# Performance work log

Hardware: AMD Instinct MI355X
Metric: run time of the kernel (lower is better)

Reference implementation:

```python
import jax, jax.numpy as jnp
import numpy as np

B, T, N, D, H, MH = 4, 16, 128, 16, 64, 128  # batch, timesteps, nodes, n_in_node, n_hid, msg_hid


def setup_inputs() -> dict:
    key = jax.random.key(0)
    ks = jax.random.split(key, 24)
    s = 0.1
    inp = {
        'A': jax.random.uniform(ks[0], (B, N, N), dtype=jnp.float32),
        'X': jax.random.normal(ks[1], (B, T, N, D), dtype=jnp.float32),
        'W_msg1': s * jax.random.normal(ks[2], (2 * H, MH), dtype=jnp.float32),
        'b_msg1': s * jax.random.normal(ks[3], (MH,), dtype=jnp.float32),
        'W_msg2': s * jax.random.normal(ks[4], (MH, H), dtype=jnp.float32),
        'b_msg2': s * jax.random.normal(ks[5], (H,), dtype=jnp.float32),
        'W_ir': s * jax.random.normal(ks[6], (D, H), dtype=jnp.float32),
        'b_ir': s * jax.random.normal(ks[7], (H,), dtype=jnp.float32),
        'W_ii': s * jax.random.normal(ks[8], (D, H), dtype=jnp.float32),
        'b_ii': s * jax.random.normal(ks[9], (H,), dtype=jnp.float32),
        'W_in': s * jax.random.normal(ks[10], (D, H), dtype=jnp.float32),
        'b_in': s * jax.random.normal(ks[11], (H,), dtype=jnp.float32),
        'W_hr': s * jax.random.normal(ks[12], (H, H), dtype=jnp.float32),
        'W_hi': s * jax.random.normal(ks[13], (H, H), dtype=jnp.float32),
        'W_hh': s * jax.random.normal(ks[14], (H, H), dtype=jnp.float32),
        'W_o1': s * jax.random.normal(ks[15], (H, H), dtype=jnp.float32),
        'b_o1': s * jax.random.normal(ks[16], (H,), dtype=jnp.float32),
        'W_o2': s * jax.random.normal(ks[17], (H, H), dtype=jnp.float32),
        'b_o2': s * jax.random.normal(ks[18], (H,), dtype=jnp.float32),
        'W_o3': s * jax.random.normal(ks[19], (H, D), dtype=jnp.float32),
        'b_o3': s * jax.random.normal(ks[20], (D,), dtype=jnp.float32),
        'log_sigma': jnp.log(jnp.float32(0.1)),
    }
    return inp


def reference(A, X, W_msg1, b_msg1, W_msg2, b_msg2, W_ir, b_ir, W_ii, b_ii,
              W_in, b_in, W_hr, W_hi, W_hh, W_o1, b_o1, W_o2, b_o2, W_o3,
              b_o3, log_sigma):
    Bv, Tv, Nv, Dv = X.shape
    Hv = W_hr.shape[0]
    # project_adjacency: symmetrize, zero diag, clamp to [0,1]
    A = (A + jnp.swapaxes(A, -1, -2)) * 0.5
    A = A * (1.0 - jnp.eye(Nv, dtype=A.dtype))
    A = jnp.clip(A, 0.0, 1.0)
    # split msg_fc1 into sender / receiver halves (cat([senders, receivers]) @ W)
    W1s, W1r = W_msg1[:Hv], W_msg1[Hv:]

    def step(carry, xs):
        hidden, total = carry
        x_t, x_next = xs  # [B,N,D]
        # message passing on hidden state: msg1[b,i,j] = tanh(h_i@W1s + h_j@W1r + b)
        hs = hidden @ W1s                      # [B,N,MH] sender part
        hr = hidden @ W1r + b_msg1             # [B,N,MH] receiver part
        m1 = jnp.tanh(hs[:, :, None, :] + hr[:, None, :, :])  # [B,N,N,MH]
        msg = jnp.tanh(m1 @ W_msg2 + b_msg2)   # [B,N,N,H]
        # weight by soft adjacency, sum over senders i -> agg at receiver j
        agg = jnp.einsum('bij,bijh->bjh', A, msg)  # [B,N,H]
        # GRU-style gating
        r = jax.nn.sigmoid(x_t @ W_ir + b_ir + agg @ W_hr)
        i = jax.nn.sigmoid(x_t @ W_ii + b_ii + agg @ W_hi)
        n = jnp.tanh(x_t @ W_in + b_in + r * (agg @ W_hh))
        hidden_new = (1.0 - i) * n + i * hidden
        # output MLP with residual
        p1 = jax.nn.relu(hidden_new @ W_o1 + b_o1)
        p2 = jax.nn.relu(p1 @ W_o2 + b_o2)
        pred = x_t + (p2 @ W_o3 + b_o3)
        # gaussian log-likelihood
        sigma = jnp.exp(log_sigma)
        mse = jnp.sum((x_next - pred) ** 2)
        const = Nv * Dv * Bv * jnp.log(sigma * jnp.sqrt(2.0 * jnp.pi))
        total = total - (mse / (2.0 * sigma ** 2) + const)
        return (hidden_new, total), pred

    hidden0 = jnp.zeros((Bv, Nv, Hv), dtype=X.dtype)
    xs = (jnp.swapaxes(X[:, :-1], 0, 1), jnp.swapaxes(X[:, 1:], 0, 1))  # time-major
    (_, loglik), preds = jax.lax.scan(step, (hidden0, jnp.float32(0.0)), xs)
    X_pred = jnp.swapaxes(preds, 0, 1)  # [B, T-1, N, D]
    return X_pred, loglik
```

## Files before the change

kernel.cpp:

```cpp
#include <hip/hip_runtime.h>

#define NBLK 512

#define OFF_HS   0
#define OFF_PART 65536
#define OFF_SYNC 66048
#define OFF_BF   66560

#define BW2F 0
#define BWIR 8192
#define BWII 9216
#define BWIN 10240
#define BWHR 11264
#define BWHI 15360
#define BWHH 19456
#define BWO1 23552
#define BWO2 27648
#define BWO3 31744
#define BW1S 32768

#define INIT_TOTAL (32768 + 512 + 49152)

typedef __attribute__((ext_vector_type(8))) __bf16 bf16x8;
typedef __attribute__((ext_vector_type(4))) float f32x4;
union frag_u { bf16x8 v; unsigned short s[8]; int4 q; };
union ldu { int4 q; unsigned short s[8]; };

__device__ __forceinline__ unsigned short f2b(float x) {
  unsigned int u = __float_as_uint(x);
  u += 0x7fffu + ((u >> 16) & 1u);
  return (unsigned short)(u >> 16);
}
__device__ __forceinline__ float b2f(unsigned short u) {
  return __uint_as_float(((unsigned int)u) << 16);
}
__device__ __forceinline__ float fast_tanh(float x) {
  float e = __builtin_amdgcn_exp2f(x * 2.8853900817779268f);
  return 1.0f - 2.0f * __builtin_amdgcn_rcpf(e + 1.0f);
}
__device__ __forceinline__ float fast_sigmoid(float x) {
  float e = __builtin_amdgcn_exp2f(x * -1.4426950408889634f);
  return __builtin_amdgcn_rcpf(1.0f + e);
}
__device__ __forceinline__ void st_coh_u32(unsigned* p, unsigned v) {
  __hip_atomic_store(p, v, __ATOMIC_RELAXED, __HIP_MEMORY_SCOPE_AGENT);
}
__device__ __forceinline__ void st_coh_i32(int* p, int v) {
  __hip_atomic_store(p, v, __ATOMIC_RELAXED, __HIP_MEMORY_SCOPE_AGENT);
}

__global__ void init_kernel(const float* __restrict__ W_msg2,
                            const float* __restrict__ W_ir, const float* __restrict__ W_ii,
                            const float* __restrict__ W_in,
                            const float* __restrict__ W_hr, const float* __restrict__ W_hi,
                            const float* __restrict__ W_hh,
                            const float* __restrict__ W_o1, const float* __restrict__ W_o2,
                            const float* __restrict__ W_o3,
                            const float* __restrict__ W_msg1, float* __restrict__ ws) {
  int idx = blockIdx.x * 256 + threadIdx.x;
  unsigned short* bw = (unsigned short*)(ws + OFF_BF);
  if (idx < 32768) { ws[OFF_HS + idx] = 0.0f; return; }
  idx -= 32768;
  if (idx < 512) { ((int*)(ws + OFF_SYNC))[idx] = 0; return; }
  idx -= 512;
  if (idx < 8192) {
    int f = idx >> 9, l = (idx >> 3) & 63, jj = idx & 7;
    int kc = f >> 2, nt = f & 3;
    int k = kc * 32 + ((l >> 4) << 3) + jj;
    int n = (nt << 4) + (l & 15);
    bw[BW2F + idx] = f2b(W_msg2[k * 64 + n]);
    return;
  }
  idx -= 8192;
  if (idx < 1024) { bw[BWIR + idx] = f2b(W_ir[idx]); return; }
  idx -= 1024;
  if (idx < 1024) { bw[BWII + idx] = f2b(W_ii[idx]); return; }
  idx -= 1024;
  if (idx < 1024) { bw[BWIN + idx] = f2b(W_in[idx]); return; }
  idx -= 1024;
  if (idx < 4096) { bw[BWHR + idx] = f2b(W_hr[idx]); return; }
  idx -= 4096;
  if (idx < 4096) { bw[BWHI + idx] = f2b(W_hi[idx]); return; }
  idx -= 4096;
  if (idx < 4096) { bw[BWHH + idx] = f2b(W_hh[idx]); return; }
  idx -= 4096;
  if (idx < 4096) { bw[BWO1 + idx] = f2b(W_o1[idx]); return; }
  idx -= 4096;
  if (idx < 4096) { bw[BWO2 + idx] = f2b(W_o2[idx]); return; }
  idx -= 4096;
  if (idx < 1024) { bw[BWO3 + idx] = f2b(W_o3[idx]); return; }
  idx -= 1024;
  if (idx < 16384) { bw[BW1S + idx] = f2b(W_msg1[idx]); return; }
}

__launch_bounds__(256, 2)
__global__ void step_all_kernel(const float* __restrict__ A, const float* __restrict__ X,
                                const float* __restrict__ b_msg1, const float* __restrict__ b_msg2,
                                const float* __restrict__ b_ir, const float* __restrict__ b_ii,
                                const float* __restrict__ b_in,
                                const float* __restrict__ b_o1, const float* __restrict__ b_o2,
                                const float* __restrict__ b_o3,
                                float* __restrict__ ws, float* __restrict__ out) {
  const int tid = threadIdx.x;
  const int bj = blockIdx.x;
  const int b = bj >> 7, j = bj & 127;
  const int wave = tid >> 6, lane = tid & 63;
  const unsigned short* bw = (const unsigned short*)(ws + OFF_BF);
  unsigned short* hs16 = (unsigned short*)(ws + OFF_HS);
  int* flags = (int*)(ws + OFF_SYNC);

  __shared__ unsigned short lds_gate[12288];
  __shared__ unsigned short lds_w1[16384];
  __shared__ unsigned short lds_out[9216];
  __shared__ __align__(16) float sh_hr[128];
  __shared__ __align__(16) float sh_Ar[128];
  __shared__ float sh_aggw[4][64];
  __shared__ float sh_agg[64];
  __shared__ float sh_x[16];
  __shared__ float sh_hid[64];
  __shared__ float sh_pre[4][64];
  __shared__ int sh_w01;

  {
    const int4* src = (const int4*)(bw + BWHR);
    int4* dst = (int4*)lds_gate;
    for (int i = tid; i < 1536; i += 256) dst[i] = src[i];
    const int4* s2 = (const int4*)(bw + BW1S);
    int4* d2 = (int4*)lds_w1;
    for (int i = tid; i < 2048; i += 256) d2[i] = s2[i];
    const int4* s3 = (const int4*)(bw + BWO1);
    int4* d3 = (int4*)lds_out;
    for (int i = tid; i < 1152; i += 256) d3[i] = s3[i];
  }
  if (tid < 128) {
    float a1 = A[(b << 14) + (j << 7) + tid];
    float a2 = A[(b << 14) + (tid << 7) + j];
    float v = 0.5f * (a1 + a2);
    v = (tid == j) ? 0.0f : v;
    sh_Ar[tid] = fminf(fmaxf(v, 0.0f), 1.0f);
    sh_hr[tid] = b_msg1[tid];
  } else if (tid < 192) {
    sh_hid[tid - 128] = 0.0f;
  }
  if (tid == 0) sh_w01 = 0;

  frag_u Bf[16];
  const int4* bw2 = (const int4*)bw;
#pragma unroll
  for (int f = 0; f < 16; ++f) Bf[f].q = bw2[f * 64 + lane];
  float b2v[4];
#pragma unroll
  for (int nt = 0; nt < 4; ++nt) b2v[nt] = b_msg2[nt * 16 + (lane & 15)];
  float my_bias = 0.0f;
  if (wave == 0) my_bias = b_ir[lane];
  else if (wave == 1) my_bias = b_ii[lane];
  else if (wave == 3) my_bias = b_in[lane];
  const float bm1a = b_msg1[lane], bm1b = b_msg1[lane + 64];
  const float bo1 = b_o1[lane], bo2 = b_o2[lane];
  const float bo3 = (lane < 16) ? b_o3[lane] : 0.0f;
  float macc = 0.0f;

  const int lane15 = lane & 15;
  const int k0 = (lane >> 4) << 3;
  __syncthreads();

  for (int t = 0; t < 15; ++t) {
    const int par = t & 1;
    const unsigned short* hs_cur = hs16 + par * 65536;
    unsigned short* hs_nxt = hs16 + (par ^ 1) * 65536;

    if (tid < 16) sh_x[tid] = X[(((b << 4) + t) << 11) + (j << 4) + tid];

    ldu va[8];
    {
      const unsigned short* p0 = hs_cur + (((b << 7) + (wave << 5) + lane15) << 7) + k0;
      const unsigned short* p1 = p0 + 2048;
      asm volatile(
          "global_load_dwordx4 %0, %8, off sc0 sc1\n\t"
          "global_load_dwordx4 %1, %8, off offset:64 sc0 sc1\n\t"
          "global_load_dwordx4 %2, %8, off offset:128 sc0 sc1\n\t"
          "global_load_dwordx4 %3, %8, off offset:192 sc0 sc1\n\t"
          "global_load_dwordx4 %4, %9, off sc0 sc1\n\t"
          "global_load_dwordx4 %5, %9, off offset:64 sc0 sc1\n\t"
          "global_load_dwordx4 %6, %9, off offset:128 sc0 sc1\n\t"
          "global_load_dwordx4 %7, %9, off offset:192 sc0 sc1\n\t"
          "s_waitcnt vmcnt(0)"
          : "=&v"(va[0].q), "=&v"(va[1].q), "=&v"(va[2].q), "=&v"(va[3].q),
            "=&v"(va[4].q), "=&v"(va[5].q), "=&v"(va[6].q), "=&v"(va[7].q)
          : "v"(p0), "v"(p1)
          : "memory");
    }

    float part[4] = {0.f, 0.f, 0.f, 0.f};
#pragma unroll
    for (int c = 0; c < 2; ++c) {
      f32x4 acc[4];
#pragma unroll
      for (int nt = 0; nt < 4; ++nt) acc[nt] = (f32x4){0.f, 0.f, 0.f, 0.f};
#pragma unroll
      for (int kc = 0; kc < 4; ++kc) {
        const ldu& u = va[c * 4 + kc];
        const float* hp = sh_hr + kc * 32 + k0;
        frag_u Af;
#pragma unroll
        for (int e = 0; e < 8; ++e)
          Af.s[e] = f2b(fast_tanh(b2f(u.s[e]) + hp[e]));
#pragma unroll
        for (int nt = 0; nt < 4; ++nt)
          acc[nt] = __builtin_amdgcn_mfma_f32_16x16x32_bf16(Af.v, Bf[kc * 4 + nt].v, acc[nt], 0, 0, 0);
      }
      const int ibase = ((wave << 1) + c) << 4;
      float4 aw = *(const float4*)(sh_Ar + ibase + ((lane >> 4) << 2));
#pragma unroll
      for (int r = 0; r < 4; ++r) {
        float wv = (r == 0) ? aw.x : (r == 1) ? aw.y : (r == 2) ? aw.z : aw.w;
#pragma unroll
        for (int nt = 0; nt < 4; ++nt)
          part[nt] += wv * fast_tanh(acc[nt][r] + b2v[nt]);
      }
    }
#pragma unroll
    for (int nt = 0; nt < 4; ++nt) {
      part[nt] += __shfl_xor(part[nt], 16);
      part[nt] += __shfl_xor(part[nt], 32);
    }
    if (lane < 16) {
#pragma unroll
      for (int nt = 0; nt < 4; ++nt) sh_aggw[wave][nt * 16 + lane] = part[nt];
    }
    __syncthreads();
    if (tid < 64)
      sh_agg[tid] = sh_aggw[0][tid] + sh_aggw[1][tid] + sh_aggw[2][tid] + sh_aggw[3][tid];
    __syncthreads();

    {
      const int h = lane;
      float s = my_bias;
      if (wave == 3) {
#pragma unroll
        for (int d = 0; d < 16; ++d) s += sh_x[d] * b2f(bw[BWIN + d * 64 + h]);
      } else {
        if (wave < 2) {
          const int xoff = (wave == 0) ? BWIR : BWII;
#pragma unroll
          for (int d = 0; d < 16; ++d) s += sh_x[d] * b2f(bw[xoff + d * 64 + h]);
        }
        const int woff = wave * 4096;
        for (int k = 0; k < 64; ++k) s += sh_agg[k] * b2f(lds_gate[woff + k * 64 + h]);
      }
      sh_pre[wave][h] = s;
    }
    __syncthreads();
    if (tid < 64) {
      float r  = fast_sigmoid(sh_pre[0][tid]);
      float ig = fast_sigmoid(sh_pre[1][tid]);
      float n  = fast_tanh(sh_pre[3][tid] + r * sh_pre[2][tid]);
      sh_hid[tid] = (1.0f - ig) * n + ig * sh_hid[tid];
    }
    __syncthreads();

    if (wave == 3) {
      float s = bo1;
      for (int k = 0; k < 64; ++k) s += sh_hid[k] * b2f(lds_out[k * 64 + lane]);
      sh_pre[0][lane] = fmaxf(s, 0.0f);
      s = bo2;
      for (int k = 0; k < 64; ++k) s += sh_pre[0][k] * b2f(lds_out[4096 + k * 64 + lane]);
      sh_pre[1][lane] = fmaxf(s, 0.0f);
      if (lane < 16) {
        float s3 = bo3;
        for (int k = 0; k < 64; ++k) s3 += sh_pre[1][k] * b2f(lds_out[8192 + (k << 4) + lane]);
        float pred = sh_x[lane] + s3;
        out[((b * 15 + t) * 128 + j) * 16 + lane] = pred;
        float d = X[(((b << 4) + t + 1) << 11) + (j << 4) + lane] - pred;
        macc += d * d;
      }
    } else if (t < 14) {
      if (wave <= 1) {
        const int m = tid;
        float s = 0.0f;
        for (int h = 0; h < 64; ++h) s += sh_hid[h] * b2f(lds_w1[h * 128 + m]);
        float hi = __shfl_down(s, 1);
        if (!(lane & 1)) {
          unsigned pk = ((unsigned)f2b(hi) << 16) | (unsigned)f2b(s);
          st_coh_u32((unsigned*)hs_nxt + (bj << 6) + (m >> 1), pk);
        }
        asm volatile("s_waitcnt vmcnt(0)" ::: "memory");
        if (lane == 0) atomicAdd(&sh_w01, 1);
        if (wave == 0) {
          const int tgt = t + 1;
          if (lane == 0) {
            while (__hip_atomic_load(&sh_w01, __ATOMIC_RELAXED, __HIP_MEMORY_SCOPE_WORKGROUP) < 2 * tgt) {}
            st_coh_i32(flags + (b << 7) + j, tgt);
          }
          const int* fp = flags + (b << 7) + (lane << 1);
          int2 fv;
          do {
            asm volatile("global_load_dwordx2 %0, %1, off sc0 sc1\n\ts_waitcnt vmcnt(0)"
                         : "=v"(fv) : "v"(fp) : "memory");
          } while (__any(fv.x < tgt || fv.y < tgt));
        }
      } else {
        float s1 = bm1a, s2 = bm1b;
        for (int h = 0; h < 64; ++h) {
          float hv = sh_hid[h];
          s1 += hv * b2f(lds_w1[8192 + h * 128 + lane]);
          s2 += hv * b2f(lds_w1[8192 + h * 128 + lane + 64]);
        }
        sh_hr[lane] = s1;
        sh_hr[lane + 64] = s2;
      }
    }
    __syncthreads();
  }

  if (wave == 3) {
    macc += __shfl_xor(macc, 1);
    macc += __shfl_xor(macc, 2);
    macc += __shfl_xor(macc, 4);
    macc += __shfl_xor(macc, 8);
    if (lane == 0) ws[OFF_PART + bj] = macc;
  }
}

__global__ void final_kernel(const float* __restrict__ log_sigma, const float* __restrict__ ws,
                             float* __restrict__ out) {
  __shared__ float red[256];
  const int tid = threadIdx.x;
  red[tid] = ws[OFF_PART + tid] + ws[OFF_PART + 256 + tid];
  __syncthreads();
  if (tid == 0) {
    float mse = 0.0f;
    for (int i = 0; i < 256; ++i) mse += red[i];
    float sigma = expf(log_sigma[0]);
    float cst = 8192.0f * logf(sigma * sqrtf(6.2831853071795864f));
    out[122880] = -(mse / (2.0f * sigma * sigma) + 15.0f * cst);
  }
}

extern "C" void kernel_launch(void* const* d_in, const int* in_sizes, int n_in,
                              void* d_out, int out_size, void* d_ws, size_t ws_size,
                              hipStream_t stream) {
  (void)in_sizes; (void)n_in; (void)out_size; (void)ws_size;
  const float* A      = (const float*)d_in[0];
  const float* X      = (const float*)d_in[1];
  const float* W_msg1 = (const float*)d_in[2];
  const float* b_msg1 = (const float*)d_in[3];
  const float* W_msg2 = (const float*)d_in[4];
  const float* b_msg2 = (const float*)d_in[5];
  const float* W_ir   = (const float*)d_in[6];
  const float* b_ir   = (const float*)d_in[7];
  const float* W_ii   = (const float*)d_in[8];
  const float* b_ii   = (const float*)d_in[9];
  const float* W_in   = (const float*)d_in[10];
  const float* b_in   = (const float*)d_in[11];
  const float* W_hr   = (const float*)d_in[12];
  const float* W_hi   = (const float*)d_in[13];
  const float* W_hh   = (const float*)d_in[14];
  const float* W_o1   = (const float*)d_in[15];
  const float* b_o1   = (const float*)d_in[16];
  const float* W_o2   = (const float*)d_in[17];
  const float* b_o2   = (const float*)d_in[18];
  const float* W_o3   = (const float*)d_in[19];
  const float* b_o3   = (const float*)d_in[20];
  const float* log_sigma = (const float*)d_in[21];
  float* ws  = (float*)d_ws;
  float* out = (float*)d_out;

  init_kernel<<<(INIT_TOTAL + 255) / 256, 256, 0, stream>>>(
      W_msg2, W_ir, W_ii, W_in, W_hr, W_hi, W_hh, W_o1, W_o2, W_o3, W_msg1, ws);
  step_all_kernel<<<NBLK, 256, 0, stream>>>(A, X, b_msg1, b_msg2, b_ir, b_ii, b_in,
                                            b_o1, b_o2, b_o3, ws, out);
  final_kernel<<<1, 256, 0, stream>>>(log_sigma, ws, out);
}
```

Before: 281.2 us.

## Transpose LDS weights, prefold tanh scale, preload X and vectorize small matvecs

Stores the gate, msg1 and output weights transposed in LDS with padded rows, so each lane reads contiguous ushort4 chunks and accumulates into four partial sums. The tanh input scale is folded into W_msg2, b_msg2, b_msg1 and the stored hidden projections, which removes a multiply per tanh in the hot message loop. Bf16 packing now uses a single perm instruction. All X timesteps are preloaded into shared memory once and the input weights are kept in registers, removing per-step global loads. The receiver-side msg1 projection reads a transposed global copy instead of LDS, and the new pack rounds ties differently from the old rounding, which adds small numeric drift.

```diff
diff --git a/kernel.cpp b/kernel.cpp
--- a/kernel.cpp
+++ b/kernel.cpp
@@ -1,30 +1,32 @@
 #include <hip/hip_runtime.h>
 
 #define NBLK 512
+#define CSCALE 2.8853900817779268f
 
 #define OFF_HS   0
 #define OFF_PART 65536
 #define OFF_SYNC 66048
 #define OFF_BF   66560
 
-#define BW2F 0
-#define BWIR 8192
-#define BWII 9216
-#define BWIN 10240
-#define BWHR 11264
-#define BWHI 15360
-#define BWHH 19456
-#define BWO1 23552
-#define BWO2 27648
-#define BWO3 31744
-#define BW1S 32768
-
-#define INIT_TOTAL (32768 + 512 + 49152)
+#define BW2F  0
+#define BWIR  8192
+#define BWII  9216
+#define BWIN  10240
+#define BWHR  11264
+#define BWHI  15360
+#define BWHH  19456
+#define BWO1  23552
+#define BWO2  27648
+#define BWO3  31744
+#define BW1S  32768
+#define BW1RT 49152
+
+#define INIT_TOTAL (32768 + 512 + 49152 + 8192)
 
 typedef __attribute__((ext_vector_type(8))) __bf16 bf16x8;
 typedef __attribute__((ext_vector_type(4))) float f32x4;
 union frag_u { bf16x8 v; unsigned short s[8]; int4 q; };
-union ldu { int4 q; unsigned short s[8]; };
+union ldu { int4 q; unsigned short s[8]; unsigned u[4]; };
 
 __device__ __forceinline__ unsigned short f2b(float x) {
   unsigned int u = __float_as_uint(x);
@@ -35,12 +37,21 @@
   return __uint_as_float(((unsigned int)u) << 16);
 }
 __device__ __forceinline__ float fast_tanh(float x) {
-  float e = __builtin_amdgcn_exp2f(x * 2.8853900817779268f);
+  float e = __builtin_amdgcn_exp2f(x * CSCALE);
+  return 1.0f - 2.0f * __builtin_amdgcn_rcpf(e + 1.0f);
+}
+__device__ __forceinline__ float tanh_pre(float x) {
+  float e = __builtin_amdgcn_exp2f(x);
   return 1.0f - 2.0f * __builtin_amdgcn_rcpf(e + 1.0f);
 }
 __device__ __forceinline__ float fast_sigmoid(float x) {
   float e = __builtin_amdgcn_exp2f(x * -1.4426950408889634f);
   return __builtin_amdgcn_rcpf(1.0f + e);
+}
+__device__ __forceinline__ unsigned pack_bf2(float lo, float hi) {
+  unsigned a = __float_as_uint(lo) + 0x8000u;
+  unsigned b = __float_as_uint(hi) + 0x8000u;
+  return __builtin_amdgcn_perm(b, a, 0x07060302u);
 }
 __device__ __forceinline__ void st_coh_u32(unsigned* p, unsigned v) {
   __hip_atomic_store(p, v, __ATOMIC_RELAXED, __HIP_MEMORY_SCOPE_AGENT);
@@ -68,7 +79,7 @@
     int kc = f >> 2, nt = f & 3;
     int k = kc * 32 + ((l >> 4) << 3) + jj;
     int n = (nt << 4) + (l & 15);
-    bw[BW2F + idx] = f2b(W_msg2[k * 64 + n]);
+    bw[BW2F + idx] = f2b(W_msg2[k * 64 + n] * CSCALE);
     return;
   }
   idx -= 8192;
@@ -91,6 +102,12 @@
   if (idx < 1024) { bw[BWO3 + idx] = f2b(W_o3[idx]); return; }
   idx -= 1024;
   if (idx < 16384) { bw[BW1S + idx] = f2b(W_msg1[idx]); return; }
+  idx -= 16384;
+  if (idx < 8192) {
+    int m = idx >> 6, h = idx & 63;
+    bw[BW1RT + idx] = f2b(W_msg1[(64 + h) * 128 + m]);
+    return;
+  }
 }
 
 __launch_bounds__(256, 2)
@@ -109,28 +126,37 @@
   unsigned short* hs16 = (unsigned short*)(ws + OFF_HS);
   int* flags = (int*)(ws + OFF_SYNC);
 
-  __shared__ unsigned short lds_gate[12288];
-  __shared__ unsigned short lds_w1[16384];
-  __shared__ unsigned short lds_out[9216];
+  __shared__ __align__(16) unsigned short lds_gate_t[3 * 64 * 68];
+  __shared__ __align__(16) unsigned short lds_w1t[128 * 68];
+  __shared__ __align__(16) unsigned short lds_outt[2 * 64 * 68 + 16 * 68];
   __shared__ __align__(16) float sh_hr[128];
   __shared__ __align__(16) float sh_Ar[128];
-  __shared__ float sh_aggw[4][64];
-  __shared__ float sh_agg[64];
-  __shared__ float sh_x[16];
-  __shared__ float sh_hid[64];
-  __shared__ float sh_pre[4][64];
+  __shared__ __align__(16) float sh_aggw[4][64];
+  __shared__ __align__(16) float sh_agg[64];
+  __shared__ __align__(16) float sh_xall[256];
+  __shared__ __align__(16) float sh_hid[64];
+  __shared__ __align__(16) float sh_pre[4][64];
   __shared__ int sh_w01;
 
+  for (int i = tid; i < 12288; i += 256) {
+    int g = i >> 12, r = i & 4095, k = r >> 6, h = r & 63;
+    lds_gate_t[g * 4352 + h * 68 + k] = bw[BWHR + i];
+  }
+  for (int i = tid; i < 8192; i += 256) {
+    int h = i >> 7, m = i & 127;
+    lds_w1t[m * 68 + h] = bw[BW1S + i];
+  }
+  for (int i = tid; i < 8192; i += 256) {
+    int o = i >> 12, r = i & 4095, k = r >> 6, h = r & 63;
+    lds_outt[o * 4352 + h * 68 + k] = bw[BWO1 + i];
+  }
+  for (int i = tid; i < 1024; i += 256) {
+    int k = i >> 4, d = i & 15;
+    lds_outt[8704 + d * 68 + k] = bw[BWO3 + i];
+  }
   {
-    const int4* src = (const int4*)(bw + BWHR);
-    int4* dst = (int4*)lds_gate;
-    for (int i = tid; i < 1536; i += 256) dst[i] = src[i];
-    const int4* s2 = (const int4*)(bw + BW1S);
-    int4* d2 = (int4*)lds_w1;
-    for (int i = tid; i < 2048; i += 256) d2[i] = s2[i];
-    const int4* s3 = (const int4*)(bw + BWO1);
-    int4* d3 = (int4*)lds_out;
-    for (int i = tid; i < 1152; i += 256) d3[i] = s3[i];
+    int t0 = tid >> 4, d = tid & 15;
+    sh_xall[tid] = X[(((b << 4) + t0) << 11) + (j << 4) + d];
   }
   if (tid < 128) {
     float a1 = A[(b << 14) + (j << 7) + tid];
@@ -138,7 +164,7 @@
     float v = 0.5f * (a1 + a2);
     v = (tid == j) ? 0.0f : v;
     sh_Ar[tid] = fminf(fmaxf(v, 0.0f), 1.0f);
-    sh_hr[tid] = b_msg1[tid];
+    sh_hr[tid] = b_msg1[tid] * CSCALE;
   } else if (tid < 192) {
     sh_hid[tid - 128] = 0.0f;
   }
@@ -150,11 +176,15 @@
   for (int f = 0; f < 16; ++f) Bf[f].q = bw2[f * 64 + lane];
   float b2v[4];
 #pragma unroll
-  for (int nt = 0; nt < 4; ++nt) b2v[nt] = b_msg2[nt * 16 + (lane & 15)];
+  for (int nt = 0; nt < 4; ++nt) b2v[nt] = b_msg2[nt * 16 + (lane & 15)] * CSCALE;
   float my_bias = 0.0f;
-  if (wave == 0) my_bias = b_ir[lane];
-  else if (wave == 1) my_bias = b_ii[lane];
-  else if (wave == 3) my_bias = b_in[lane];
+  float wx[16];
+  if (wave != 2) {
+    my_bias = (wave == 0) ? b_ir[lane] : (wave == 1) ? b_ii[lane] : b_in[lane];
+    const int xo = (wave == 0) ? BWIR : (wave == 1) ? BWII : BWIN;
+#pragma unroll
+    for (int d = 0; d < 16; ++d) wx[d] = b2f(bw[xo + d * 64 + lane]);
+  }
   const float bm1a = b_msg1[lane], bm1b = b_msg1[lane + 64];
   const float bo1 = b_o1[lane], bo2 = b_o2[lane];
   const float bo3 = (lane < 16) ? b_o3[lane] : 0.0f;
@@ -168,8 +198,6 @@
     const int par = t & 1;
     const unsigned short* hs_cur = hs16 + par * 65536;
     unsigned short* hs_nxt = hs16 + (par ^ 1) * 65536;
-
-    if (tid < 16) sh_x[tid] = X[(((b << 4) + t) << 11) + (j << 4) + tid];
 
     ldu va[8];
     {
@@ -202,9 +230,14 @@
         const ldu& u = va[c * 4 + kc];
         const float* hp = sh_hr + kc * 32 + k0;
         frag_u Af;
-#pragma unroll
-        for (int e = 0; e < 8; ++e)
-          Af.s[e] = f2b(fast_tanh(b2f(u.s[e]) + hp[e]));
+        int* ap = (int*)&Af.q;
+#pragma unroll
+        for (int p = 0; p < 4; ++p) {
+          unsigned w = u.u[p];
+          float x0 = __uint_as_float(w << 16) + hp[2 * p];
+          float x1 = __uint_as_float(w & 0xffff0000u) + hp[2 * p + 1];
+          ap[p] = (int)pack_bf2(tanh_pre(x0), tanh_pre(x1));
+        }
 #pragma unroll
         for (int nt = 0; nt < 4; ++nt)
           acc[nt] = __builtin_amdgcn_mfma_f32_16x16x32_bf16(Af.v, Bf[kc * 4 + nt].v, acc[nt], 0, 0, 0);
@@ -216,7 +249,7 @@
         float wv = (r == 0) ? aw.x : (r == 1) ? aw.y : (r == 2) ? aw.z : aw.w;
 #pragma unroll
         for (int nt = 0; nt < 4; ++nt)
-          part[nt] += wv * fast_tanh(acc[nt][r] + b2v[nt]);
+          part[nt] += wv * tanh_pre(acc[nt][r] + b2v[nt]);
       }
     }
 #pragma unroll
@@ -234,21 +267,30 @@
     __syncthreads();
 
     {
-      const int h = lane;
-      float s = my_bias;
-      if (wave == 3) {
-#pragma unroll
-        for (int d = 0; d < 16; ++d) s += sh_x[d] * b2f(bw[BWIN + d * 64 + h]);
-      } else {
-        if (wave < 2) {
-          const int xoff = (wave == 0) ? BWIR : BWII;
-#pragma unroll
-          for (int d = 0; d < 16; ++d) s += sh_x[d] * b2f(bw[xoff + d * 64 + h]);
-        }
-        const int woff = wave * 4096;
-        for (int k = 0; k < 64; ++k) s += sh_agg[k] * b2f(lds_gate[woff + k * 64 + h]);
-      }
-      sh_pre[wave][h] = s;
+      float s = 0.0f;
+      if (wave != 2) {
+        s = my_bias;
+        const float4* xr = (const float4*)(sh_xall + (t << 4));
+#pragma unroll
+        for (int c = 0; c < 4; ++c) {
+          float4 xv = xr[c];
+          s += xv.x * wx[4 * c] + xv.y * wx[4 * c + 1] + xv.z * wx[4 * c + 2] + xv.w * wx[4 * c + 3];
+        }
+      }
+      if (wave != 3) {
+        const ushort4* row = (const ushort4*)(lds_gate_t + wave * 4352 + lane * 68);
+        const float4* ag = (const float4*)sh_agg;
+        float a0 = s, a1 = 0.f, a2 = 0.f, a3 = 0.f;
+#pragma unroll
+        for (int c = 0; c < 16; ++c) {
+          ushort4 wv = row[c];
+          float4 av = ag[c];
+          a0 += av.x * b2f(wv.x); a1 += av.y * b2f(wv.y);
+          a2 += av.z * b2f(wv.z); a3 += av.w * b2f(wv.w);
+        }
+        s = (a0 + a1) + (a2 + a3);
+      }
+      sh_pre[wave][lane] = s;
     }
     __syncthreads();
     if (tid < 64) {
@@ -260,30 +302,61 @@
     __syncthreads();
 
     if (wave == 3) {
-      float s = bo1;
-      for (int k = 0; k < 64; ++k) s += sh_hid[k] * b2f(lds_out[k * 64 + lane]);
-      sh_pre[0][lane] = fmaxf(s, 0.0f);
-      s = bo2;
-      for (int k = 0; k < 64; ++k) s += sh_pre[0][k] * b2f(lds_out[4096 + k * 64 + lane]);
-      sh_pre[1][lane] = fmaxf(s, 0.0f);
+      const float4* h4 = (const float4*)sh_hid;
+      {
+        const ushort4* r1 = (const ushort4*)(lds_outt + lane * 68);
+        float a0 = bo1, a1 = 0.f, a2 = 0.f, a3 = 0.f;
+#pragma unroll
+        for (int c = 0; c < 16; ++c) {
+          ushort4 wv = r1[c]; float4 hv = h4[c];
+          a0 += hv.x * b2f(wv.x); a1 += hv.y * b2f(wv.y);
+          a2 += hv.z * b2f(wv.z); a3 += hv.w * b2f(wv.w);
+        }
+        sh_pre[0][lane] = fmaxf((a0 + a1) + (a2 + a3), 0.0f);
+      }
+      {
+        const ushort4* r2 = (const ushort4*)(lds_outt + 4352 + lane * 68);
+        const float4* p4 = (const float4*)sh_pre[0];
+        float a0 = bo2, a1 = 0.f, a2 = 0.f, a3 = 0.f;
+#pragma unroll
+        for (int c = 0; c < 16; ++c) {
+          ushort4 wv = r2[c]; float4 pv = p4[c];
+          a0 += pv.x * b2f(wv.x); a1 += pv.y * b2f(wv.y);
+          a2 += pv.z * b2f(wv.z); a3 += pv.w * b2f(wv.w);
+        }
+        sh_pre[1][lane] = fmaxf((a0 + a1) + (a2 + a3), 0.0f);
+      }
       if (lane < 16) {
-        float s3 = bo3;
-        for (int k = 0; k < 64; ++k) s3 += sh_pre[1][k] * b2f(lds_out[8192 + (k << 4) + lane]);
-        float pred = sh_x[lane] + s3;
+        const ushort4* r3 = (const ushort4*)(lds_outt + 8704 + lane * 68);
+        const float4* q4 = (const float4*)sh_pre[1];
+        float a0 = bo3, a1 = 0.f, a2 = 0.f, a3 = 0.f;
+#pragma unroll
+        for (int c = 0; c < 16; ++c) {
+          ushort4 wv = r3[c]; float4 qv = q4[c];
+          a0 += qv.x * b2f(wv.x); a1 += qv.y * b2f(wv.y);
+          a2 += qv.z * b2f(wv.z); a3 += qv.w * b2f(wv.w);
+        }
+        float pred = sh_xall[(t << 4) + lane] + (a0 + a1) + (a2 + a3);
         out[((b * 15 + t) * 128 + j) * 16 + lane] = pred;
-        float d = X[(((b << 4) + t + 1) << 11) + (j << 4) + lane] - pred;
+        float d = sh_xall[((t + 1) << 4) + lane] - pred;
         macc += d * d;
       }
     } else if (t < 14) {
       if (wave <= 1) {
         const int m = tid;
-        float s = 0.0f;
-        for (int h = 0; h < 64; ++h) s += sh_hid[h] * b2f(lds_w1[h * 128 + m]);
+        const ushort4* row = (const ushort4*)(lds_w1t + m * 68);
+        const float4* h4 = (const float4*)sh_hid;
+        float a0 = 0.f, a1 = 0.f, a2 = 0.f, a3 = 0.f;
+#pragma unroll
+        for (int c = 0; c < 16; ++c) {
+          ushort4 wv = row[c]; float4 hv = h4[c];
+          a0 += hv.x * b2f(wv.x); a1 += hv.y * b2f(wv.y);
+          a2 += hv.z * b2f(wv.z); a3 += hv.w * b2f(wv.w);
+        }
+        float s = ((a0 + a1) + (a2 + a3)) * CSCALE;
         float hi = __shfl_down(s, 1);
-        if (!(lane & 1)) {
-          unsigned pk = ((unsigned)f2b(hi) << 16) | (unsigned)f2b(s);
-          st_coh_u32((unsigned*)hs_nxt + (bj << 6) + (m >> 1), pk);
-        }
+        if (!(lane & 1))
+          st_coh_u32((unsigned*)hs_nxt + (bj << 6) + (m >> 1), pack_bf2(s, hi));
         asm volatile("s_waitcnt vmcnt(0)" ::: "memory");
         if (lane == 0) atomicAdd(&sh_w01, 1);
         if (wave == 0) {
@@ -300,14 +373,25 @@
           } while (__any(fv.x < tgt || fv.y < tgt));
         }
       } else {
-        float s1 = bm1a, s2 = bm1b;
-        for (int h = 0; h < 64; ++h) {
-          float hv = sh_hid[h];
-          s1 += hv * b2f(lds_w1[8192 + h * 128 + lane]);
-          s2 += hv * b2f(lds_w1[8192 + h * 128 + lane + 64]);
-        }
-        sh_hr[lane] = s1;
-        sh_hr[lane + 64] = s2;
+        const int4* wp1 = (const int4*)(bw + BW1RT + (lane << 6));
+        const int4* wp2 = (const int4*)(bw + BW1RT + ((lane + 64) << 6));
+        const float4* h4 = (const float4*)sh_hid;
+        float s1a = bm1a, s1b = 0.f, s2a = bm1b, s2b = 0.f;
+#pragma unroll
+        for (int c = 0; c < 8; ++c) {
+          ldu u1, u2; u1.q = wp1[c]; u2.q = wp2[c];
+          float4 h0 = h4[2 * c], h1 = h4[2 * c + 1];
+          s1a += h0.x * b2f(u1.s[0]); s1b += h0.y * b2f(u1.s[1]);
+          s1a += h0.z * b2f(u1.s[2]); s1b += h0.w * b2f(u1.s[3]);
+          s1a += h1.x * b2f(u1.s[4]); s1b += h1.y * b2f(u1.s[5]);
+          s1a += h1.z * b2f(u1.s[6]); s1b += h1.w * b2f(u1.s[7]);
+          s2a += h0.x * b2f(u2.s[0]); s2b += h0.y * b2f(u2.s[1]);
+          s2a += h0.z * b2f(u2.s[2]); s2b += h0.w * b2f(u2.s[3]);
+          s2a += h1.x * b2f(u2.s[4]); s2b += h1.y * b2f(u2.s[5]);
+          s2a += h1.z * b2f(u2.s[6]); s2b += h1.w * b2f(u2.s[7]);
+        }
+        sh_hr[lane] = (s1a + s1b) * CSCALE;
+        sh_hr[lane + 64] = (s2a + s2b) * CSCALE;
       }
     }
     __syncthreads();
```

Measured after the change: 262.9 us. -6.5%, faster.
